# Performance work log

Measured on AMD Instinct MI355X. Metric: run time of the kernel, lower is better.

## Reference

```python
import jax, jax.numpy as jnp
import numpy as np

N_HEAD, D_MODEL, D_HEAD = 16, 1024, 64
BSZ, QLEN, KLEN = 4, 1024, 2048
MEM_LEN = KLEN - QLEN


def _rel_shift(x):
    # x: [b, q, k, n] -> Transformer-XL relative shift
    b, q, k, n = x.shape
    zero_pad = jnp.zeros((b, q, 1, n), dtype=x.dtype)
    x_padded = jnp.concatenate([zero_pad, x], axis=2)        # [b, q, k+1, n]
    x_padded = x_padded.reshape(b, k + 1, q, n)
    return x_padded[:, 1:].reshape(b, q, k, n)


def setup_inputs() -> dict:
    key = jax.random.key(0)
    ks = jax.random.split(key, 8)
    s = 0.02
    w = jax.random.normal(ks[0], (BSZ, KLEN, D_MODEL), jnp.float32)
    r = jax.random.normal(ks[1], (1, KLEN, D_MODEL), jnp.float32)
    r_w_bias = jax.random.normal(ks[2], (N_HEAD, D_HEAD), jnp.float32) * s
    r_r_bias = jax.random.normal(ks[3], (N_HEAD, D_HEAD), jnp.float32) * s
    Wq = jax.random.normal(ks[4], (D_MODEL, N_HEAD * D_HEAD), jnp.float32) * s
    Wkv = jax.random.normal(ks[5], (D_MODEL, 2 * N_HEAD * D_HEAD), jnp.float32) * s
    Wr = jax.random.normal(ks[6], (D_MODEL, N_HEAD * D_HEAD), jnp.float32) * s
    Wo = jax.random.normal(ks[7], (N_HEAD * D_HEAD, D_MODEL), jnp.float32) * s
    # causal mask with memory: query i attends to j <= i + MEM_LEN
    attn_mask = jnp.triu(jnp.ones((QLEN, KLEN), dtype=bool), k=MEM_LEN + 1)
    return {"w": w, "r": r, "r_w_bias": r_w_bias, "r_r_bias": r_r_bias,
            "Wq": Wq, "Wkv": Wkv, "Wr": Wr, "Wo": Wo,
            "attn_mask": attn_mask, "qlen": QLEN}


def reference(w, r, r_w_bias, r_r_bias, Wq, Wkv, Wr, Wo, attn_mask, qlen):
    bsz, klen, _ = w.shape
    rlen = r.shape[1]
    scale = 1.0 / (D_HEAD ** 0.5)

    q = (w[:, -qlen:] @ Wq).reshape(bsz, qlen, N_HEAD, D_HEAD)
    kv = w @ Wkv
    k, v = jnp.split(kv, 2, axis=-1)
    k = k.reshape(bsz, klen, N_HEAD, D_HEAD)
    v = v.reshape(bsz, klen, N_HEAD, D_HEAD)
    rk = (r[0] @ Wr).reshape(rlen, N_HEAD, D_HEAD)

    AC = jnp.einsum('bind,bjnd->bijn', q + r_w_bias, k)
    BD = jnp.einsum('bind,jnd->bijn', q + r_r_bias, rk)
    attn_score = (AC + _rel_shift(BD)) * scale
    attn_score = jnp.where(attn_mask[None, :, :, None], jnp.float32(-1e30), attn_score)
    attn_prob = jax.nn.softmax(attn_score, axis=2)
    attn_vec = jnp.einsum('bijn,bjnd->bind', attn_prob, v)
    attn_vec = attn_vec.reshape(bsz, qlen, N_HEAD * D_HEAD)
    return attn_vec @ Wo
```

## Files before the change

kernel.cpp:

```cpp
#include <hip/hip_runtime.h>

constexpr int BSZ  = 4;
constexpr int NH   = 16;
constexpr int DH   = 64;
constexpr int QL   = 1024;
constexpr int KLN  = 2048;
constexpr int DM   = 1024;
constexpr int MEM  = 1024;

typedef __bf16 bf16x8  __attribute__((ext_vector_type(8)));
typedef __bf16 bf16x4t __attribute__((ext_vector_type(4)));
typedef float  f32x4   __attribute__((ext_vector_type(4)));

__device__ __forceinline__ void g2l16(__bf16* lds, const __bf16* g) {
    __builtin_amdgcn_global_load_lds(
        (const __attribute__((address_space(1))) unsigned int*)g,
        (__attribute__((address_space(3))) unsigned int*)lds, 16, 0, 0);
}

__global__ __launch_bounds__(256)
void prep(const float* __restrict__ w, const float* __restrict__ r,
          const float* __restrict__ Wq, const float* __restrict__ Wr,
          const float* __restrict__ Wo, const float* __restrict__ Wkv,
          __bf16* __restrict__ wbh, __bf16* __restrict__ rbh,
          __bf16* __restrict__ WqT, __bf16* __restrict__ WrT,
          __bf16* __restrict__ WoT, __bf16* __restrict__ WkvT)
{
    __shared__ __bf16 t[64 * 72];
    const int id = blockIdx.x;
    if (id < 5120) {
        const float* in; __bf16* out; size_t i;
        if (id < 4096) { in = w; out = wbh; i = ((size_t)id * 256 + threadIdx.x) * 8; }
        else { in = r; out = rbh; i = ((size_t)(id - 4096) * 256 + threadIdx.x) * 8; }
        float4 a = *(const float4*)(in + i);
        float4 b = *(const float4*)(in + i + 4);
        bf16x8 y = {(__bf16)a.x, (__bf16)a.y, (__bf16)a.z, (__bf16)a.w,
                    (__bf16)b.x, (__bf16)b.y, (__bf16)b.z, (__bf16)b.w};
        *(bf16x8*)(out + i) = y;
        return;
    }
    const int tt = id - 5120;
    const int z = tt >> 9, rem = tt & 511;
    const int xx = rem & 31, yy = rem >> 5;
    const float* in; __bf16* out; int N;
    if (z == 0)      { in = Wq;  out = WqT;  N = 1024; }
    else if (z == 1) { in = Wr;  out = WrT;  N = 1024; }
    else if (z == 2) { in = Wo;  out = WoT;  N = 1024; }
    else             { in = Wkv; out = WkvT; N = 2048; }
    if (xx * 64 >= N) return;
    const int n0 = xx * 64, k0 = yy * 64;
    const int row = threadIdx.x >> 2, seg = (threadIdx.x & 3) << 4;
    const float* src = in + (long)(k0 + row) * N + n0 + seg;
#pragma unroll
    for (int u = 0; u < 16; u += 4) {
        float4 x = *(const float4*)(src + u);
        t[(seg + u + 0) * 72 + row] = (__bf16)x.x;
        t[(seg + u + 1) * 72 + row] = (__bf16)x.y;
        t[(seg + u + 2) * 72 + row] = (__bf16)x.z;
        t[(seg + u + 3) * 72 + row] = (__bf16)x.w;
    }
    __syncthreads();
    __bf16* dst = out + (long)(n0 + row) * 1024 + k0 + seg;
    *(uint4*)(dst)     = *(const uint4*)(t + row * 72 + seg);
    *(uint4*)(dst + 8) = *(const uint4*)(t + row * 72 + seg + 8);
}

__device__ __forceinline__ void gemm_core(
    const __bf16* __restrict__ A, const __bf16* __restrict__ BT,
    __bf16* As, __bf16* Bs, int m0, int n0, int K, f32x4 (&acc)[4][4])
{
    const int tid = threadIdx.x, w = tid >> 6, l = tid & 63;
    const int il = l & 15, quad = l >> 4;
    const int wm = (w >> 1) * 64, wn = (w & 1) * 64;
    const int lr = l >> 2, kc = (l & 3) ^ (lr & 3);

    const __bf16* ag = A  + (long)(m0 + w * 32 + lr) * K + kc * 8;
    const __bf16* bg = BT + (long)(n0 + w * 32 + lr) * K + kc * 8;
    __bf16* al0 = As + (w * 32) * 32;
    __bf16* al1 = As + (w * 32 + 16) * 32;
    __bf16* bl0 = Bs + (w * 32) * 32;
    __bf16* bl1 = Bs + (w * 32 + 16) * 32;
    const int rsw = il & 3;

    for (int k0 = 0; k0 < K; k0 += 32) {
        __syncthreads();
        g2l16(al0, ag + k0);
        g2l16(al1, ag + k0 + 16 * K);
        g2l16(bl0, bg + k0);
        g2l16(bl1, bg + k0 + 16 * K);
        __syncthreads();

        bf16x8 af[4], bf[4];
#pragma unroll
        for (int f = 0; f < 4; ++f) {
            af[f] = *(const bf16x8*)(As + (wm + f * 16 + il) * 32 + ((quad ^ rsw) << 3));
            bf[f] = *(const bf16x8*)(Bs + (wn + f * 16 + il) * 32 + ((quad ^ rsw) << 3));
        }
#pragma unroll
        for (int i = 0; i < 4; ++i)
#pragma unroll
            for (int j = 0; j < 4; ++j)
                acc[i][j] = __builtin_amdgcn_mfma_f32_16x16x32_bf16(
                    af[i], bf[j], acc[i][j], 0, 0, 0);
    }
}

__global__ __launch_bounds__(256, 2)
void gemm_proj(const __bf16* __restrict__ wbh, const __bf16* __restrict__ rbh,
               const __bf16* __restrict__ WqT, const __bf16* __restrict__ WkvT,
               const __bf16* __restrict__ WrT,
               __bf16* __restrict__ qwh, __bf16* __restrict__ qrh,
               __bf16* __restrict__ kh, __bf16* __restrict__ vhT,
               __bf16* __restrict__ rkh,
               const float* __restrict__ bw, const float* __restrict__ br)
{
    __shared__ __bf16 As[128 * 32];
    __shared__ __bf16 Bs[128 * 32];
    const int id = blockIdx.x;
    const __bf16 *A, *BT;
    int m0, n0, zz, kind;
    if (id < 1024) {
        n0 = (id & 15) * 128; m0 = ((id >> 4) & 15) * 128; zz = id >> 8;
        A = wbh + (size_t)zz * KLN * DM; BT = WkvT; kind = 3;
    } else if (id < 1280) {
        const int t = id - 1024;
        n0 = (t & 7) * 128; m0 = ((t >> 3) & 7) * 128; zz = t >> 6;
        A = wbh + (size_t)zz * KLN * DM + (size_t)MEM * DM; BT = WqT; kind = 2;
    } else {
        const int t = id - 1280;
        n0 = (t & 7) * 128; m0 = (t >> 3) * 128; zz = 0;
        A = rbh; BT = WrT; kind = 4;
    }

    f32x4 acc[4][4] = {};
    gemm_core(A, BT, As, Bs, m0, n0, DM, acc);

    const int tid = threadIdx.x, w = tid >> 6, l = tid & 63;
    const int il = l & 15, quad = l >> 4;
    const int wm = (w >> 1) * 64, wn = (w & 1) * 64;

    if (kind == 2) {
#pragma unroll
        for (int j = 0; j < 4; ++j) {
            const int col = n0 + wn + j * 16 + il;
            const int hn = col >> 6, d = col & 63;
            const float bwv = bw[col], brv = br[col];
            __bf16* q1 = qwh + ((size_t)(zz * 16 + hn) * 1024) * 64 + d;
            __bf16* q2 = qrh + ((size_t)(zz * 16 + hn) * 1024) * 64 + d;
#pragma unroll
            for (int i = 0; i < 4; ++i) {
                const int mb = m0 + wm + i * 16 + quad * 4;
#pragma unroll
                for (int rr = 0; rr < 4; ++rr) {
                    float v = acc[i][j][rr];
                    q1[(size_t)(mb + rr) * 64] = (__bf16)(v + bwv);
                    q2[(size_t)(mb + rr) * 64] = (__bf16)(v + brv);
                }
            }
        }
    } else if (kind == 3) {
        if (n0 + wn < 1024) {
#pragma unroll
            for (int j = 0; j < 4; ++j) {
                const int col = n0 + wn + j * 16 + il;
                const int hn = col >> 6, d = col & 63;
                __bf16* kp = kh + ((size_t)(zz * 16 + hn) * 2048) * 64 + d;
#pragma unroll
                for (int i = 0; i < 4; ++i) {
                    const int mb = m0 + wm + i * 16 + quad * 4;
#pragma unroll
                    for (int rr = 0; rr < 4; ++rr)
                        kp[(size_t)(mb + rr) * 64] = (__bf16)acc[i][j][rr];
                }
            }
        } else {
#pragma unroll
            for (int j = 0; j < 4; ++j) {
                const int col = n0 + wn + j * 16 + il - 1024;
                const int hn = col >> 6, d = col & 63;
                __bf16* vp = vhT + ((size_t)((zz * 16 + hn) * 64 + d)) * 2048;
#pragma unroll
                for (int i = 0; i < 4; ++i) {
                    const int mb = m0 + wm + i * 16 + quad * 4;
                    bf16x4t pk = {(__bf16)acc[i][j][0], (__bf16)acc[i][j][1],
                                  (__bf16)acc[i][j][2], (__bf16)acc[i][j][3]};
                    *(bf16x4t*)(vp + mb) = pk;
                }
            }
        }
    } else {
#pragma unroll
        for (int j = 0; j < 4; ++j) {
            const int col = n0 + wn + j * 16 + il;
            const int hn = col >> 6, d = col & 63;
            __bf16* rp = rkh + ((size_t)hn * 2048) * 64 + d;
#pragma unroll
            for (int i = 0; i < 4; ++i) {
                const int mb = m0 + wm + i * 16 + quad * 4;
#pragma unroll
                for (int rr = 0; rr < 4; ++rr)
                    rp[(size_t)(mb + rr) * 64] = (__bf16)acc[i][j][rr];
            }
        }
    }
}

__global__ __launch_bounds__(256, 2)
void gemm_out(const __bf16* __restrict__ avh, const __bf16* __restrict__ WoT,
              float* __restrict__ C)
{
    __shared__ __bf16 As[128 * 32];
    __shared__ __bf16 Bs[128 * 32];
    const int zz = blockIdx.z;
    const __bf16* A = avh + (size_t)zz * QL * DM;
    const int m0 = blockIdx.y * 128, n0 = blockIdx.x * 128;

    f32x4 acc[4][4] = {};
    gemm_core(A, WoT, As, Bs, m0, n0, DM, acc);

    const int tid = threadIdx.x, w = tid >> 6, l = tid & 63;
    const int il = l & 15, quad = l >> 4;
    const int wm = (w >> 1) * 64, wn = (w & 1) * 64;
    float* Cb = C + (size_t)zz * QL * DM;
#pragma unroll
    for (int i = 0; i < 4; ++i)
#pragma unroll
        for (int j = 0; j < 4; ++j) {
            float* cp = Cb + (long)(m0 + wm + i * 16 + quad * 4) * DM
                           + n0 + wn + j * 16 + il;
#pragma unroll
            for (int rr = 0; rr < 4; ++rr) cp[(long)rr * DM] = acc[i][j][rr];
        }
}

__global__ __launch_bounds__(256, 2)
void attn_mfma(const __bf16* __restrict__ qwh, const __bf16* __restrict__ qrh,
               const __bf16* __restrict__ kh, const __bf16* __restrict__ vhT,
               const __bf16* __restrict__ rkh, float* __restrict__ Op,
               float* __restrict__ ml)
{
    extern __shared__ __bf16 smem[];
    __bf16* kt  = smem;
    __bf16* vt  = smem + 4096;
    __bf16* rkt = smem + 8192;
    float*  scf = (float*)(smem + 20480);

    const int bx = blockIdx.x;
    const int part = bx & 1;
    const int bx2 = bx >> 1;
    const int ib = (bx2 & 1) ? (7 - (bx2 >> 1)) : (bx2 >> 1);
    const int i0 = ib * 128;
    const int n = blockIdx.y, b = blockIdx.z;
    const int tid = threadIdx.x;
    const int w = tid >> 6, l = tid & 63;
    const int il = l & 15, quad = l >> 4;
    const int iw0 = i0 + w * 32;

    bf16x8 qwf[2][2], qrf[2][2];
#pragma unroll
    for (int g = 0; g < 2; ++g) {
        const size_t qoff =
            ((size_t)((b * 16 + n) * QL + iw0 + 16 * g + il)) * 64 + quad * 8;
        qwf[g][0] = *(const bf16x8*)(qwh + qoff);
        qwf[g][1] = *(const bf16x8*)(qwh + qoff + 32);
        qrf[g][0] = *(const bf16x8*)(qrh + qoff);
        qrf[g][1] = *(const bf16x8*)(qrh + qoff + 32);
    }

    f32x4 O[2][4] = {};
    float m_i[2] = {-1e30f, -1e30f}, l_i[2] = {0.f, 0.f};
    const float c = 0.125f * 1.44269504f;

    const int srow = l >> 3, scl = l & 7;
    const __bf16* kbase  = kh  + ((size_t)((b * 16 + n) * KLN)) * 64;
    const __bf16* vbase0 = vhT + ((size_t)((b * 16 + n) * 64)) * KLN;
    const __bf16* rbp    = rkh + ((size_t)(n * KLN)) * 64;

    const int xk0 = ((quad) ^ (il & 7)) << 3;
    const int xk1 = ((quad + 4) ^ (il & 7)) << 3;

    const int nt = 2 * ib + 18;
    const int t0 = (part * nt) / 2;
    const int t1 = ((part + 1) * nt) / 2;
    int rot = (t0 % 3) * 64;

    const int ubB = 96 - 32 * w;

    for (int jt = t0; jt < t1; ++jt) {
        const int j0 = jt * 64;
        const int vu0 = j0 - i0 + 896;
        __syncthreads();
#pragma unroll
        for (int it = 0; it < 2; ++it) {
            const int row = w * 16 + it * 8 + srow;
            g2l16(kt + (w * 16 + it * 8) * 64,
                  kbase + ((size_t)(j0 + row)) * 64 + ((scl ^ srow) << 3));
        }
#pragma unroll
        for (int it = 0; it < 2; ++it) {
            const int row = w * 16 + it * 8 + srow;
            g2l16(vt + (w * 16 + it * 8) * 64,
                  vbase0 + (size_t)row * KLN + j0 + ((scl ^ srow) << 3));
        }
        if (jt == t0) {
#pragma unroll
            for (int it = 0; it < 6; ++it) {
                const int lbase = w * 48 + it * 8;
                int pb = lbase + rot; if (pb >= 192) pb -= 192;
                int vu = vu0 + lbase + srow;
                vu = vu < 0 ? 0 : (vu > KLN - 1 ? KLN - 1 : vu);
                g2l16(rkt + pb * 64,
                      rbp + (size_t)vu * 64 + ((scl ^ srow) << 3));
            }
        } else {
#pragma unroll
            for (int it = 0; it < 2; ++it) {
                const int lbase = 128 + w * 16 + it * 8;
                int pb = lbase + rot; if (pb >= 192) pb -= 192;
                int vu = vu0 + lbase + srow;
                vu = vu < 0 ? 0 : (vu > KLN - 1 ? KLN - 1 : vu);
                g2l16(rkt + pb * 64,
                      rbp + (size_t)vu * 64 + ((scl ^ srow) << 3));
            }
        }
        __syncthreads();

        const bool edge = (j0 + 63 > i0 + MEM);

        f32x4 sf[2][4];
#pragma unroll
        for (int fr = 0; fr < 4; ++fr) {
            const __bf16* ka = kt + (fr * 16 + il) * 64;
            bf16x8 a0 = *(const bf16x8*)(ka + xk0);
            bf16x8 a1 = *(const bf16x8*)(ka + xk1);
            __builtin_amdgcn_s_setprio(1);
#pragma unroll
            for (int g = 0; g < 2; ++g) {
                f32x4 acc = {};
                acc = __builtin_amdgcn_mfma_f32_16x16x32_bf16(a0, qwf[g][0], acc, 0, 0, 0);
                acc = __builtin_amdgcn_mfma_f32_16x16x32_bf16(a1, qwf[g][1], acc, 0, 0, 0);
                sf[g][fr] = acc;
            }
            __builtin_amdgcn_s_setprio(0);
        }

        bf16x8 ra[6][2];
#pragma unroll
        for (int uf2 = 0; uf2 < 6; ++uf2) {
            int pr = ubB + uf2 * 16 + il + rot; if (pr >= 192) pr -= 192;
            const __bf16* rp_ = rkt + pr * 64;
            ra[uf2][0] = *(const bf16x8*)(rp_ + xk0);
            ra[uf2][1] = *(const bf16x8*)(rp_ + xk1);
        }
        bf16x8 va[4][2];
#pragma unroll
        for (int df = 0; df < 4; ++df) {
            const __bf16* vp_ = vt + (df * 16 + il) * 64;
            va[df][0] = *(const bf16x8*)(vp_ + xk0);
            va[df][1] = *(const bf16x8*)(vp_ + xk1);
        }

        float* scw = scf + w * 1344;
#pragma unroll
        for (int g = 0; g < 2; ++g) {
#pragma unroll
            for (int uf = 0; uf < 5; ++uf) {
                const int idx = uf + 1 - g;
                f32x4 acc = {};
                __builtin_amdgcn_s_setprio(1);
                acc = __builtin_amdgcn_mfma_f32_16x16x32_bf16(ra[idx][0], qrf[g][0], acc, 0, 0, 0);
                acc = __builtin_amdgcn_mfma_f32_16x16x32_bf16(ra[idx][1], qrf[g][1], acc, 0, 0, 0);
                __builtin_amdgcn_s_setprio(0);
                *(f32x4*)(scw + il * 84 + uf * 16 + quad * 4) = acc;
            }

            const int i_gl = iw0 + 16 * g + il;
            float sv[4][4];
            float tmax = -1e30f;
#pragma unroll
            for (int fr = 0; fr < 4; ++fr) {
                const int base = il * 83 + fr * 16 + quad * 4 + 15;
#pragma unroll
                for (int rr = 0; rr < 4; ++rr) {
                    const int jl_ = fr * 16 + quad * 4 + rr;
                    float s = sf[g][fr][rr] + scw[base + rr];
                    if (edge) s = (j0 + jl_ > i_gl + MEM) ? -1e30f : s;
                    sv[fr][rr] = s;
                    tmax = fmaxf(tmax, s);
                }
            }
            tmax = fmaxf(tmax, __shfl_xor(tmax, 16));
            tmax = fmaxf(tmax, __shfl_xor(tmax, 32));
            const float m_new = fmaxf(m_i[g], tmax);
            const float alpha = exp2f((m_i[g] - m_new) * c);
            float psum = 0.f;
            __bf16* prow = (__bf16*)(scw + il * 84);
#pragma unroll
            for (int fr = 0; fr < 4; ++fr) {
                bf16x4t p4;
#pragma unroll
                for (int rr = 0; rr < 4; ++rr) {
                    float p = exp2f((sv[fr][rr] - m_new) * c);
                    psum += p;
                    p4[rr] = (__bf16)p;
                }
                *(bf16x4t*)(prow + fr * 16 + quad * 4) = p4;
            }
            psum += __shfl_xor(psum, 16);
            psum += __shfl_xor(psum, 32);
            l_i[g] = l_i[g] * alpha + psum;
            m_i[g] = m_new;
#pragma unroll
            for (int df = 0; df < 4; ++df) O[g][df] *= alpha;

            bf16x8 p0 = *(const bf16x8*)(prow + quad * 8);
            bf16x8 p1 = *(const bf16x8*)(prow + 32 + quad * 8);
            __builtin_amdgcn_s_setprio(1);
#pragma unroll
            for (int df = 0; df < 4; ++df) {
                O[g][df] = __builtin_amdgcn_mfma_f32_16x16x32_bf16(va[df][0], p0, O[g][df], 0, 0, 0);
                O[g][df] = __builtin_amdgcn_mfma_f32_16x16x32_bf16(va[df][1], p1, O[g][df], 0, 0, 0);
            }
            __builtin_amdgcn_s_setprio(0);
        }
        rot += 64; if (rot >= 192) rot -= 192;
    }

#pragma unroll
    for (int g = 0; g < 2; ++g) {
        const int iL = w * 32 + 16 * g + il;
        float* opb = Op + (size_t)part * 4194304
                        + ((((size_t)b * NH + n) * 8 + ib)) * 8192
                        + (size_t)iL * 64 + quad * 4;
#pragma unroll
        for (int df = 0; df < 4; ++df)
            *(f32x4*)(opb + df * 16) = O[g][df];
        if (quad == 0) {
            const size_t base = (((size_t)b * NH + n) * 8 + ib) * 128 + iL;
            ml[(size_t)part * 65536 + base]          = m_i[g];
            ml[131072 + (size_t)part * 65536 + base] = l_i[g];
        }
    }
}

__global__ __launch_bounds__(256)
void attn_combine(const float* __restrict__ Op, const float* __restrict__ ml,
                  __bf16* __restrict__ av)
{
    const int tid = threadIdx.x;
    const int i = blockIdx.x * 4 + (tid >> 6);
    const int d = tid & 63;
    const int n = blockIdx.y, b = blockIdx.z;
    const int ib = i >> 7, iL = i & 127;
    const float c = 0.125f * 1.44269504f;

    const size_t mb = (((size_t)b * NH + n) * 8 + ib) * 128 + iL;
    const float m0 = ml[mb], m1 = ml[mb + 65536];
    const float l0 = ml[131072 + mb], l1 = ml[131072 + 65536 + mb];
    const float ms = fmaxf(m0, m1);
    const float w0 = exp2f((m0 - ms) * c);
    const float w1 = exp2f((m1 - ms) * c);
    const float ls = w0 * l0 + w1 * l1;

    const size_t ob = (((size_t)b * NH + n) * 8 + ib) * 8192
                      + (size_t)iL * 64 + d;
    const float o = w0 * Op[ob] + w1 * Op[ob + 4194304];
    av[((size_t)(b * QL + i)) * DM + n * 64 + d] = (__bf16)(o / ls);
}

extern "C" void kernel_launch(void* const* d_in, const int* in_sizes, int n_in,
                              void* d_out, int out_size, void* d_ws, size_t ws_size,
                              hipStream_t stream)
{
    const float* w   = (const float*)d_in[0];
    const float* r   = (const float*)d_in[1];
    const float* bwb = (const float*)d_in[2];
    const float* brb = (const float*)d_in[3];
    const float* Wq  = (const float*)d_in[4];
    const float* Wkv = (const float*)d_in[5];
    const float* Wr  = (const float*)d_in[6];
    const float* Wo  = (const float*)d_in[7];
    float* out = (float*)d_out;

    char* ws = (char*)d_ws;
    __bf16* wbh  = (__bf16*)(ws);
    __bf16* rbh  = (__bf16*)(ws + ((size_t)16 << 20));
    __bf16* WqT  = (__bf16*)(ws + ((size_t)20 << 20));
    __bf16* WkvT = (__bf16*)(ws + ((size_t)22 << 20));
    __bf16* WrT  = (__bf16*)(ws + ((size_t)26 << 20));
    __bf16* WoT  = (__bf16*)(ws + ((size_t)28 << 20));
    __bf16* qwh  = (__bf16*)(ws + ((size_t)30 << 20));
    __bf16* qrh  = (__bf16*)(ws + ((size_t)38 << 20));
    __bf16* kh   = (__bf16*)(ws + ((size_t)46 << 20));
    __bf16* vhT  = (__bf16*)(ws + ((size_t)62 << 20));
    __bf16* rkh  = (__bf16*)(ws + ((size_t)78 << 20));
    __bf16* avh  = (__bf16*)(ws + ((size_t)82 << 20));
    float*  Op   = (float*)(ws + ((size_t)90 << 20));
    float*  mlb  = (float*)(ws + ((size_t)122 << 20));

    dim3 blk(256);
    prep<<<7168, blk, 0, stream>>>(w, r, Wq, Wr, Wo, Wkv,
                                   wbh, rbh, WqT, WrT, WoT, WkvT);
    gemm_proj<<<1408, blk, 0, stream>>>(wbh, rbh, WqT, WkvT, WrT,
                                        qwh, qrh, kh, vhT, rkh, bwb, brb);
    attn_mfma<<<dim3(16, 16, 4), blk, 62464, stream>>>(
        qwh, qrh, kh, vhT, rkh, Op, mlb);
    attn_combine<<<dim3(256, 16, 4), blk, 0, stream>>>(Op, mlb, avh);
    gemm_out<<<dim3(8, 8, 4), blk, 0, stream>>>(avh, WoT, out);
}
```

Before: 346.4 us.

## Load K, V and rk fragments directly from global, dropping LDS staging

Removes the LDS staging of K, V and rk tiles, along with the two block-wide barriers per tile, and has each wave load its MFMA operand fragments straight from global memory. The grid is also flattened to 1D with a remapping that interleaves blocks across (b, n, ib, part), probably to improve L2 locality across compute units. Shared memory drops to the score scratch only, which could allow more blocks per CU. The trade-off is that each wave now re-reads K, V and rk from global or cache without reuse across waves, and the V reads are strided.

Result: slower. 418.8 us (+20.9%).

```diff
diff --git a/kernel.cpp b/kernel.cpp
--- a/kernel.cpp
+++ b/kernel.cpp
@@ -240,17 +240,15 @@
                float* __restrict__ ml)
 {
     extern __shared__ __bf16 smem[];
-    __bf16* kt  = smem;
-    __bf16* vt  = smem + 4096;
-    __bf16* rkt = smem + 8192;
-    float*  scf = (float*)(smem + 20480);
-
-    const int bx = blockIdx.x;
-    const int part = bx & 1;
-    const int bx2 = bx >> 1;
+    float* scf = (float*)smem;
+
+    const int bid = blockIdx.x;
+    const int lin = (bid & 7) * 128 + (bid >> 3);
+    const int part = lin & 1;
+    const int bx2 = (lin >> 1) & 7;
     const int ib = (bx2 & 1) ? (7 - (bx2 >> 1)) : (bx2 >> 1);
     const int i0 = ib * 128;
-    const int n = blockIdx.y, b = blockIdx.z;
+    const int n = (lin >> 4) & 15, b = lin >> 8;
     const int tid = threadIdx.x;
     const int w = tid >> 6, l = tid & 63;
     const int il = l & 15, quad = l >> 4;
@@ -271,68 +269,27 @@
     float m_i[2] = {-1e30f, -1e30f}, l_i[2] = {0.f, 0.f};
     const float c = 0.125f * 1.44269504f;
 
-    const int srow = l >> 3, scl = l & 7;
     const __bf16* kbase  = kh  + ((size_t)((b * 16 + n) * KLN)) * 64;
     const __bf16* vbase0 = vhT + ((size_t)((b * 16 + n) * 64)) * KLN;
     const __bf16* rbp    = rkh + ((size_t)(n * KLN)) * 64;
 
-    const int xk0 = ((quad) ^ (il & 7)) << 3;
-    const int xk1 = ((quad + 4) ^ (il & 7)) << 3;
-
     const int nt = 2 * ib + 18;
     const int t0 = (part * nt) / 2;
     const int t1 = ((part + 1) * nt) / 2;
-    int rot = (t0 % 3) * 64;
 
     const int ubB = 96 - 32 * w;
 
     for (int jt = t0; jt < t1; ++jt) {
         const int j0 = jt * 64;
         const int vu0 = j0 - i0 + 896;
-        __syncthreads();
-#pragma unroll
-        for (int it = 0; it < 2; ++it) {
-            const int row = w * 16 + it * 8 + srow;
-            g2l16(kt + (w * 16 + it * 8) * 64,
-                  kbase + ((size_t)(j0 + row)) * 64 + ((scl ^ srow) << 3));
-        }
-#pragma unroll
-        for (int it = 0; it < 2; ++it) {
-            const int row = w * 16 + it * 8 + srow;
-            g2l16(vt + (w * 16 + it * 8) * 64,
-                  vbase0 + (size_t)row * KLN + j0 + ((scl ^ srow) << 3));
-        }
-        if (jt == t0) {
-#pragma unroll
-            for (int it = 0; it < 6; ++it) {
-                const int lbase = w * 48 + it * 8;
-                int pb = lbase + rot; if (pb >= 192) pb -= 192;
-                int vu = vu0 + lbase + srow;
-                vu = vu < 0 ? 0 : (vu > KLN - 1 ? KLN - 1 : vu);
-                g2l16(rkt + pb * 64,
-                      rbp + (size_t)vu * 64 + ((scl ^ srow) << 3));
-            }
-        } else {
-#pragma unroll
-            for (int it = 0; it < 2; ++it) {
-                const int lbase = 128 + w * 16 + it * 8;
-                int pb = lbase + rot; if (pb >= 192) pb -= 192;
-                int vu = vu0 + lbase + srow;
-                vu = vu < 0 ? 0 : (vu > KLN - 1 ? KLN - 1 : vu);
-                g2l16(rkt + pb * 64,
-                      rbp + (size_t)vu * 64 + ((scl ^ srow) << 3));
-            }
-        }
-        __syncthreads();
-
         const bool edge = (j0 + 63 > i0 + MEM);
 
         f32x4 sf[2][4];
 #pragma unroll
         for (int fr = 0; fr < 4; ++fr) {
-            const __bf16* ka = kt + (fr * 16 + il) * 64;
-            bf16x8 a0 = *(const bf16x8*)(ka + xk0);
-            bf16x8 a1 = *(const bf16x8*)(ka + xk1);
+            const __bf16* ka = kbase + (size_t)(j0 + fr * 16 + il) * 64 + quad * 8;
+            bf16x8 a0 = *(const bf16x8*)(ka);
+            bf16x8 a1 = *(const bf16x8*)(ka + 32);
             __builtin_amdgcn_s_setprio(1);
 #pragma unroll
             for (int g = 0; g < 2; ++g) {
@@ -347,17 +304,18 @@
         bf16x8 ra[6][2];
 #pragma unroll
         for (int uf2 = 0; uf2 < 6; ++uf2) {
-            int pr = ubB + uf2 * 16 + il + rot; if (pr >= 192) pr -= 192;
-            const __bf16* rp_ = rkt + pr * 64;
-            ra[uf2][0] = *(const bf16x8*)(rp_ + xk0);
-            ra[uf2][1] = *(const bf16x8*)(rp_ + xk1);
+            int vu = vu0 + ubB + uf2 * 16 + il;
+            vu = vu < 0 ? 0 : (vu > KLN - 1 ? KLN - 1 : vu);
+            const __bf16* rp_ = rbp + (size_t)vu * 64 + quad * 8;
+            ra[uf2][0] = *(const bf16x8*)(rp_);
+            ra[uf2][1] = *(const bf16x8*)(rp_ + 32);
         }
         bf16x8 va[4][2];
 #pragma unroll
         for (int df = 0; df < 4; ++df) {
-            const __bf16* vp_ = vt + (df * 16 + il) * 64;
-            va[df][0] = *(const bf16x8*)(vp_ + xk0);
-            va[df][1] = *(const bf16x8*)(vp_ + xk1);
+            const __bf16* vp_ = vbase0 + (size_t)(df * 16 + il) * KLN + j0 + quad * 8;
+            va[df][0] = *(const bf16x8*)(vp_);
+            va[df][1] = *(const bf16x8*)(vp_ + 32);
         }
 
         float* scw = scf + w * 1344;
@@ -423,7 +381,6 @@
             }
             __builtin_amdgcn_s_setprio(0);
         }
-        rot += 64; if (rot >= 192) rot -= 192;
     }
 
 #pragma unroll
@@ -503,7 +460,7 @@
                                    wbh, rbh, WqT, WrT, WoT, WkvT);
     gemm_proj<<<1408, blk, 0, stream>>>(wbh, rbh, WqT, WkvT, WrT,
                                         qwh, qrh, kh, vhT, rkh, bwb, brb);
-    attn_mfma<<<dim3(16, 16, 4), blk, 62464, stream>>>(
+    attn_mfma<<<1024, blk, 21504, stream>>>(
         qwh, qrh, kh, vhT, rkh, Op, mlb);
     attn_combine<<<dim3(256, 16, 4), blk, 0, stream>>>(Op, mlb, avh);
     gemm_out<<<dim3(8, 8, 4), blk, 0, stream>>>(avh, WoT, out);
```
